# Performance work log

Hardware: AMD Instinct MI355X
Metric: run time of the kernel (lower is better)

## Reference

```python
import jax, jax.numpy as jnp
import numpy as np

B, T, TA = 16, 512, 1024
D_REG, D_AUD, HID, HEADS = 512, 512, 256, 4
NREG = 4  # mouth, left_eye, right_eye, nose (dict order)
N = NREG * B * T + B * TA  # total graph nodes


def _build_edges():
    # Faithful, vectorized version of build_graph's edge construction (phoneme_times=None).
    bs = np.arange(B)[:, None]
    ts = np.arange(T)[None, :]
    src, dst = [], []
    # cross-region same-timestep edges, all ordered pairs i != j (edge_attr 0)
    for i in range(NREG):
        for j in range(NREG):
            if i != j:
                n1 = i * B * T + bs * T + ts
                n2 = j * B * T + bs * T + ts
                src.append(n1.ravel()); dst.append(n2.ravel())
    # temporal edges within each region (edge_attr 1)
    tt = np.arange(T - 1)[None, :]
    for i in range(NREG):
        n1 = i * B * T + bs * T + tt
        src.append(n1.ravel()); dst.append((n1 + 1).ravel())
    # eye (region idx 1,2) -> audio alignment edges (edge_attr 3)
    t_aud = (np.arange(T)[None, :] * TA) // T
    audio_start = NREG * B * T
    for i in (1, 2):
        n_eye = i * B * T + bs * T + ts
        n_aud = audio_start + bs * TA + t_aud
        src.append(n_eye.ravel()); dst.append(np.broadcast_to(n_aud, (B, T)).ravel())
    # self loops (PyG GATConv default add_self_loops=True)
    loops = np.arange(N)
    src.append(loops); dst.append(loops)
    return np.concatenate(src).astype(np.int32), np.concatenate(dst).astype(np.int32)


def setup_inputs() -> dict:
    key = jax.random.key(0)
    ks = iter(jax.random.split(key, 48))
    def rn(shape, scale=1.0):
        return jax.random.normal(next(ks), shape, dtype=jnp.float32) * jnp.float32(scale)
    src_np, dst_np = _build_edges()
    inp = {
        'mouth': rn((B, T, D_REG)), 'left_eye': rn((B, T, D_REG)),
        'right_eye': rn((B, T, D_REG)), 'nose': rn((B, T, D_REG)),
        'audio_embeddings': rn((B, TA, D_AUD)),
    }
    s = 1.0 / np.sqrt(D_REG)
    for name in ['mouth', 'left_eye', 'right_eye', 'nose']:
        inp['w_' + name] = rn((D_REG, HID), s)
        inp['b_' + name] = jnp.zeros((HID,), jnp.float32)
    inp['w_audio'] = rn((D_AUD, HID), 1.0 / np.sqrt(D_AUD))
    inp['b_audio'] = jnp.zeros((HID,), jnp.float32)
    # GAT layers: layer 0 in=HID, layers 1,2 in=HID*HEADS; layers 0,1 concat, layer 2 averages heads
    dims_in = [HID, HID * HEADS, HID * HEADS]
    for l, din in enumerate(dims_in):
        concat = l < 2
        inp[f'W{l}'] = rn((din, HEADS * HID), 1.0 / np.sqrt(din))
        inp[f'as{l}'] = rn((HEADS, HID), 0.1)
        inp[f'ad{l}'] = rn((HEADS, HID), 0.1)
        inp[f'bias{l}'] = jnp.zeros((HEADS * HID,) if concat else (HID,), jnp.float32)
    inp['ln_g'] = jnp.ones((HID,), jnp.float32)
    inp['ln_b'] = jnp.zeros((HID,), jnp.float32)
    inp['src'] = jnp.asarray(src_np)
    inp['dst'] = jnp.asarray(dst_np)
    return inp


def _gat(x, W, a_s, a_d, bias, src, dst, concat):
    # PyG GATConv (eval mode): gather -> per-head attention softmax over dst -> scatter-add
    H, C = a_s.shape
    h = (x @ W).reshape(-1, H, C)                      # [N,H,C]
    alpha_s = jnp.sum(h * a_s, -1)                     # [N,H]
    alpha_d = jnp.sum(h * a_d, -1)                     # [N,H]
    e = jax.nn.leaky_relu(alpha_s[src] + alpha_d[dst], 0.2)  # [E,H]
    m = jax.ops.segment_max(e, dst, num_segments=N)
    ex = jnp.exp(e - m[dst])
    denom = jax.ops.segment_sum(ex, dst, num_segments=N)
    alpha = ex / (denom[dst] + jnp.float32(1e-16))
    out = jax.ops.segment_sum(h[src] * alpha[:, :, None], dst, num_segments=N)  # [N,H,C]
    out = out.reshape(-1, H * C) if concat else out.mean(1)
    return out + bias


def _forward(mouth, left_eye, right_eye, nose, audio_embeddings,
             w_mouth, b_mouth, w_left_eye, b_left_eye, w_right_eye, b_right_eye,
             w_nose, b_nose, w_audio, b_audio,
             W0, as0, ad0, bias0, W1, as1, ad1, bias1, W2, as2, ad2, bias2,
             ln_g, ln_b, src, dst):
    x = jnp.concatenate([
        (mouth @ w_mouth + b_mouth).reshape(B * T, HID),
        (left_eye @ w_left_eye + b_left_eye).reshape(B * T, HID),
        (right_eye @ w_right_eye + b_right_eye).reshape(B * T, HID),
        (nose @ w_nose + b_nose).reshape(B * T, HID),
        (audio_embeddings @ w_audio + b_audio).reshape(B * TA, HID),
    ], axis=0)                                          # [N,HID]
    x = _gat(x, W0, as0, ad0, bias0, src, dst, True)    # [N,HID*HEADS]
    x = _gat(x, W1, as1, ad1, bias1, src, dst, True)    # [N,HID*HEADS]
    x = _gat(x, W2, as2, ad2, bias2, src, dst, False)   # [N,HID]
    mu = x.mean(-1, keepdims=True)
    var = jnp.mean(jnp.square(x - mu), -1, keepdims=True)
    x = (x - mu) / jnp.sqrt(var + jnp.float32(1e-5)) * ln_g + ln_b
    nodes_pb = NREG * T + TA
    return x.reshape(B, nodes_pb, HID).mean(1)          # [B,HID]


def reference(mouth, left_eye, right_eye, nose, audio_embeddings,
              w_mouth, b_mouth, w_left_eye, b_left_eye, w_right_eye, b_right_eye,
              w_nose, b_nose, w_audio, b_audio,
              W0, as0, ad0, bias0, W1, as1, ad1, bias1, W2, as2, ad2, bias2,
              ln_g, ln_b, src, dst):
    return _forward(mouth, left_eye, right_eye, nose, audio_embeddings,
                    w_mouth, b_mouth, w_left_eye, b_left_eye, w_right_eye, b_right_eye,
                    w_nose, b_nose, w_audio, b_audio,
                    W0, as0, ad0, bias0, W1, as1, ad1, bias1, W2, as2, ad2, bias2,
                    ln_g, ln_b, src, dst)
```

## Files before the change

kernel.cpp:

```cpp
#include <hip/hip_runtime.h>


typedef unsigned short u16;
typedef unsigned int u32;
typedef __bf16 bf16x8 __attribute__((ext_vector_type(8)));
typedef float f32x4 __attribute__((ext_vector_type(4)));

#define ASYNC16(gp, lp)                                                        \
  __builtin_amdgcn_global_load_lds(                                            \
      (const __attribute__((address_space(1))) void*)(gp),                     \
      (__attribute__((address_space(3))) void*)(lp), 16, 0, 0)

__device__ __forceinline__ u16 f2bf(float f) {
  union { float f; u32 u; } v; v.f = f;
  u32 u = v.u + 0x7FFFu + ((v.u >> 16) & 1u);
  return (u16)(u >> 16);
}
__device__ __forceinline__ float bf2f(u16 x) {
  union { u32 u; float f; } v; v.u = ((u32)x) << 16;
  return v.f;
}
__device__ __forceinline__ float4 load_bf4(const u16* p) {
  ushort4 s = *(const ushort4*)p;
  float4 r; r.x = bf2f(s.x); r.y = bf2f(s.y); r.z = bf2f(s.z); r.w = bf2f(s.w);
  return r;
}
__device__ __forceinline__ float lrelu(float v) { return v > 0.f ? v : 0.2f * v; }
__device__ __forceinline__ float dot4(float4 a, float4 b) {
  return a.x * b.x + a.y * b.y + a.z * b.z + a.w * b.w;
}
__device__ __forceinline__ float wred(float v) {
#pragma unroll
  for (int off = 32; off; off >>= 1) v += __shfl_down(v, off);
  return v;
}
__device__ __forceinline__ float wredx(float v) {
#pragma unroll
  for (int off = 32; off; off >>= 1) v += __shfl_xor(v, off);
  return v;
}

struct PK { const float* W[8]; u16* P[8]; int KB[8]; int NN[8]; int st[9]; };
__global__ __launch_bounds__(256) void pack_kernel(PK p) {
  const int f = blockIdx.x * 4 + (threadIdx.x >> 6);
  const int lane = threadIdx.x & 63;
  int e = 0;
  while (f >= p.st[e + 1]) ++e;
  const int local = f - p.st[e];
  const int KB = p.KB[e], N = p.NN[e];
  const int nt = local / KB, kb = local % KB;
  const float* W = p.W[e] + (size_t)(kb * 32 + (lane >> 4) * 8) * N + nt * 16 + (lane & 15);
  u16* dst = p.P[e] + ((size_t)local * 64 + lane) * 8;
  u16 o[8];
#pragma unroll
  for (int j = 0; j < 8; ++j) o[j] = f2bf(W[(size_t)j * N]);
  *(uint4*)dst = *(uint4*)o;
}

__global__ __launch_bounds__(256) void gemm_kernel(
    const u16* __restrict__ A, const u16* __restrict__ Bp, u16* __restrict__ C,
    int K, int ldc) {
  __shared__ __align__(16) u16 As[128 * 32];
  const int KB = K >> 5;
  const int w = blockIdx.y * 8 + blockIdx.x;
  const int xcd = w & 7, m = w >> 3;
  const int blockCol = (m & 7) * 128;
  const int blockRow = ((m >> 3) * 8 + xcd) * 128;
  const int tid = threadIdx.x;
  const int wave = tid >> 6, lane = tid & 63;
  const int wr = (wave >> 1) * 64, wc = (wave & 1) * 64;
  const int lr = lane & 15, lq = lane >> 4;
  const int sRow = wave * 16 + (lane >> 2);
  const int sGc = (lane & 3) ^ ((sRow >> 1) & 3);
  const size_t aOff0 = (size_t)(blockRow + sRow) * K + sGc * 8;
  const size_t aOff1 = aOff0 + (size_t)64 * K;
  u16* asb0 = As + wave * 512;
  u16* asb1 = As + 2048 + wave * 512;

  const u16* Bn[4];
#pragma unroll
  for (int ni = 0; ni < 4; ++ni)
    Bn[ni] = Bp + ((size_t)(((blockCol + wc) >> 4) + ni) * KB) * 512 + lane * 8;

  f32x4 acc[4][4] = {};

  for (int k0 = 0; k0 < K; k0 += 32) {
    __syncthreads();
    ASYNC16(A + aOff0 + k0, asb0);
    ASYNC16(A + aOff1 + k0, asb1);
    bf16x8 bfr[4];
#pragma unroll
    for (int ni = 0; ni < 4; ++ni)
      bfr[ni] = *(const bf16x8*)(Bn[ni] + (size_t)k0 * 16);
    __syncthreads();
    bf16x8 af[4];
#pragma unroll
    for (int mi = 0; mi < 4; ++mi) {
      const int R = wr + mi * 16 + lr;
      const int cp = lq ^ ((R >> 1) & 3);
      af[mi] = *(const bf16x8*)(&As[R * 32 + cp * 8]);
    }
#pragma unroll
    for (int mi = 0; mi < 4; ++mi)
#pragma unroll
      for (int ni = 0; ni < 4; ++ni)
        acc[mi][ni] = __builtin_amdgcn_mfma_f32_16x16x32_bf16(af[mi], bfr[ni],
                                                              acc[mi][ni], 0, 0, 0);
  }
#pragma unroll
  for (int mi = 0; mi < 4; ++mi)
#pragma unroll
    for (int ni = 0; ni < 4; ++ni) {
      const int col = blockCol + wc + ni * 16 + lr;
#pragma unroll
      for (int r = 0; r < 4; ++r) {
        const int row = blockRow + wr + mi * 16 + lq * 4 + r;
        C[(size_t)row * ldc + col] = f2bf(acc[mi][ni][r]);
      }
    }
}

struct ProjArgs { const float* x[5]; const u16* w[5]; const float* b[5]; };
__global__ __launch_bounds__(256) void proj_kernel(ProjArgs pa,
                                                   u16* __restrict__ C) {
  __shared__ __align__(16) u16 As[128 * 32];
  const int blockRow = blockIdx.y * 128, blockCol = blockIdx.x * 128;
  const int reg = blockRow >= 32768 ? 4 : (blockRow >> 13);
  const int regBase = reg == 4 ? 32768 : reg * 8192;
  const float* Af = pa.x[reg] + (size_t)(blockRow - regBase) * 512;
  const u16* Bp = pa.w[reg];
  const int tid = threadIdx.x;
  const int wave = tid >> 6, lane = tid & 63;
  const int wr = (wave >> 1) * 64, wc = (wave & 1) * 64;
  const int lr = lane & 15, lq = lane >> 4;
  const int rr = tid >> 2;
  const int cphys = tid & 3;
  const int sGc = cphys ^ ((tid >> 3) & 3);

  const u16* Bn[4];
#pragma unroll
  for (int ni = 0; ni < 4; ++ni)
    Bn[ni] = Bp + ((size_t)(((blockCol + wc) >> 4) + ni) * 16) * 512 + lane * 8;

  f32x4 acc[4][4] = {};

  for (int k0 = 0; k0 < 512; k0 += 32) {
    __syncthreads();
    bf16x8 bfr[4];
#pragma unroll
    for (int ni = 0; ni < 4; ++ni)
      bfr[ni] = *(const bf16x8*)(Bn[ni] + (size_t)k0 * 16);
#pragma unroll
    for (int i = 0; i < 2; ++i) {
      const int row = i * 64 + rr;
      const float* ap = Af + (size_t)row * 512 + k0 + sGc * 8;
      float4 f0 = *(const float4*)(ap);
      float4 f1 = *(const float4*)(ap + 4);
      uint4 pk;
      pk.x = (u32)f2bf(f0.x) | ((u32)f2bf(f0.y) << 16);
      pk.y = (u32)f2bf(f0.z) | ((u32)f2bf(f0.w) << 16);
      pk.z = (u32)f2bf(f1.x) | ((u32)f2bf(f1.y) << 16);
      pk.w = (u32)f2bf(f1.z) | ((u32)f2bf(f1.w) << 16);
      *(uint4*)(&As[row * 32 + cphys * 8]) = pk;
    }
    __syncthreads();
    bf16x8 af[4];
#pragma unroll
    for (int mi = 0; mi < 4; ++mi) {
      const int R = wr + mi * 16 + lr;
      const int cp = lq ^ ((R >> 1) & 3);
      af[mi] = *(const bf16x8*)(&As[R * 32 + cp * 8]);
    }
#pragma unroll
    for (int mi = 0; mi < 4; ++mi)
#pragma unroll
      for (int ni = 0; ni < 4; ++ni)
        acc[mi][ni] = __builtin_amdgcn_mfma_f32_16x16x32_bf16(af[mi], bfr[ni],
                                                              acc[mi][ni], 0, 0, 0);
  }
  const float* bias = pa.b[reg];
#pragma unroll
  for (int mi = 0; mi < 4; ++mi)
#pragma unroll
    for (int ni = 0; ni < 4; ++ni) {
      const int col = blockCol + wc + ni * 16 + lr;
      const float bv = bias[col];
#pragma unroll
      for (int r = 0; r < 4; ++r) {
        const int row = blockRow + wr + mi * 16 + lq * 4 + r;
        C[(size_t)row * 256 + col] = f2bf(acc[mi][ni][r] + bv);
      }
    }
}

template <bool MEAN>
__global__ __launch_bounds__(256) void agg_kernel(
    const u16* __restrict__ h, const float* __restrict__ a_s,
    const float* __restrict__ a_d, const float* __restrict__ bias,
    void* __restrict__ out) {
  const int tid = threadIdx.x;
  const int head = tid >> 6, lane = tid & 63;
  const int c4 = tid * 4;
  const float4 sa = *(const float4*)(a_s + c4);
  const float4 da = *(const float4*)(a_d + c4);
  __shared__ float asL[4][4], adL[4][4], apL[4][4];
  __shared__ float alpha[4][4][5];

  if (blockIdx.x < 8192) {
    const int bt = blockIdx.x;
    const int t = bt & 511;
    const bool hasPrev = t > 0;
    float4 hv[4], hp[4];
#pragma unroll
    for (int r = 0; r < 4; ++r)
      hv[r] = load_bf4(h + (size_t)(r * 8192 + bt) * 1024 + c4);
    if (hasPrev) {
#pragma unroll
      for (int r = 0; r < 4; ++r)
        hp[r] = load_bf4(h + (size_t)(r * 8192 + bt - 1) * 1024 + c4);
    }
#pragma unroll
    for (int r = 0; r < 4; ++r) {
      float ss = wred(dot4(hv[r], sa));
      float dd = wred(dot4(hv[r], da));
      float sp = hasPrev ? wred(dot4(hp[r], sa)) : 0.f;
      if (lane == 0) { asL[r][head] = ss; adL[r][head] = dd; apL[r][head] = sp; }
    }
    __syncthreads();
    if (tid < 16) {
      const int j = tid >> 2, hh = tid & 3;
      const float ad = adL[j][hh];
      float e[5];
#pragma unroll
      for (int r = 0; r < 4; ++r) e[r] = lrelu(asL[r][hh] + ad);
      int cnt = 4;
      if (hasPrev) { e[4] = lrelu(apL[j][hh] + ad); cnt = 5; }
      float mx = e[0];
      for (int k = 1; k < cnt; ++k) mx = fmaxf(mx, e[k]);
      float s = 0.f, ex[5];
      for (int k = 0; k < cnt; ++k) { ex[k] = __expf(e[k] - mx); s += ex[k]; }
      const float inv = 1.f / (s + 1e-16f);
#pragma unroll
      for (int k = 0; k < 5; ++k) alpha[j][hh][k] = (k < cnt) ? ex[k] * inv : 0.f;
    }
    __syncthreads();
    if constexpr (!MEAN) {
      const float4 bv = *(const float4*)(bias + c4);
      u16* ob = (u16*)out;
#pragma unroll
      for (int j = 0; j < 4; ++j) {
        const float* al = &alpha[j][head][0];
        float4 acc;
        acc.x = al[0] * hv[0].x + al[1] * hv[1].x + al[2] * hv[2].x + al[3] * hv[3].x;
        acc.y = al[0] * hv[0].y + al[1] * hv[1].y + al[2] * hv[2].y + al[3] * hv[3].y;
        acc.z = al[0] * hv[0].z + al[1] * hv[1].z + al[2] * hv[2].z + al[3] * hv[3].z;
        acc.w = al[0] * hv[0].w + al[1] * hv[1].w + al[2] * hv[2].w + al[3] * hv[3].w;
        if (hasPrev) {
          const float a4 = al[4];
          acc.x += a4 * hp[j].x; acc.y += a4 * hp[j].y;
          acc.z += a4 * hp[j].z; acc.w += a4 * hp[j].w;
        }
        ushort4 o;
        o.x = f2bf(acc.x + bv.x); o.y = f2bf(acc.y + bv.y);
        o.z = f2bf(acc.z + bv.z); o.w = f2bf(acc.w + bv.w);
        *(ushort4*)(ob + (size_t)(j * 8192 + bt) * 1024 + c4) = o;
      }
    } else {
      __shared__ float red[4][1024];
#pragma unroll
      for (int j = 0; j < 4; ++j) {
        const float* al = &alpha[j][head][0];
        float4 acc;
        acc.x = al[0] * hv[0].x + al[1] * hv[1].x + al[2] * hv[2].x + al[3] * hv[3].x;
        acc.y = al[0] * hv[0].y + al[1] * hv[1].y + al[2] * hv[2].y + al[3] * hv[3].y;
        acc.z = al[0] * hv[0].z + al[1] * hv[1].z + al[2] * hv[2].z + al[3] * hv[3].z;
        acc.w = al[0] * hv[0].w + al[1] * hv[1].w + al[2] * hv[2].w + al[3] * hv[3].w;
        if (hasPrev) {
          const float a4 = al[4];
          acc.x += a4 * hp[j].x; acc.y += a4 * hp[j].y;
          acc.z += a4 * hp[j].z; acc.w += a4 * hp[j].w;
        }
        *(float4*)(&red[j][c4]) = acc;
      }
      __syncthreads();
      const float bb = bias[tid];
      float* of = (float*)out;
#pragma unroll
      for (int j = 0; j < 4; ++j)
        of[(size_t)(j * 8192 + bt) * 256 + tid] =
            0.25f * (red[j][tid] + red[j][tid + 256] + red[j][tid + 512] +
                     red[j][tid + 768]) + bb;
    }
  } else {
    const int idx = blockIdx.x - 8192;
    const int ta = idx & 1023;
    const int node = 32768 + idx;
    const bool even = ((ta & 1) == 0);
    float4 v = load_bf4(h + (size_t)node * 1024 + c4);
    if (even) {
      const int b = idx >> 10;
      const int tt = ta >> 1;
      const int le = 8192 + b * 512 + tt;
      const int re = 16384 + b * 512 + tt;
      float4 v1 = load_bf4(h + (size_t)le * 1024 + c4);
      float4 v2 = load_bf4(h + (size_t)re * 1024 + c4);
      float s0 = wred(dot4(v, sa));
      float s1 = wred(dot4(v1, sa));
      float s2 = wred(dot4(v2, sa));
      float d0 = wred(dot4(v, da));
      if (lane == 0) {
        asL[0][head] = s0; asL[1][head] = s1; asL[2][head] = s2; adL[0][head] = d0;
      }
      __syncthreads();
      if (tid < 4) {
        const float ad = adL[0][tid];
        float e0 = lrelu(asL[0][tid] + ad);
        float e1 = lrelu(asL[1][tid] + ad);
        float e2 = lrelu(asL[2][tid] + ad);
        float mx = fmaxf(e0, fmaxf(e1, e2));
        float x0 = __expf(e0 - mx), x1 = __expf(e1 - mx), x2 = __expf(e2 - mx);
        float inv = 1.f / (x0 + x1 + x2 + 1e-16f);
        alpha[0][tid][0] = x0 * inv; alpha[0][tid][1] = x1 * inv;
        alpha[0][tid][2] = x2 * inv;
      }
      __syncthreads();
      const float a0 = alpha[0][head][0], a1 = alpha[0][head][1], a2 = alpha[0][head][2];
      v.x = a0 * v.x + a1 * v1.x + a2 * v2.x;
      v.y = a0 * v.y + a1 * v1.y + a2 * v2.y;
      v.z = a0 * v.z + a1 * v1.z + a2 * v2.z;
      v.w = a0 * v.w + a1 * v1.w + a2 * v2.w;
    }
    if constexpr (!MEAN) {
      const float4 bv = *(const float4*)(bias + c4);
      ushort4 o;
      o.x = f2bf(v.x + bv.x); o.y = f2bf(v.y + bv.y);
      o.z = f2bf(v.z + bv.z); o.w = f2bf(v.w + bv.w);
      *(ushort4*)((u16*)out + (size_t)node * 1024 + c4) = o;
    } else {
      __shared__ float redA[1024];
      *(float4*)(&redA[c4]) = v;
      __syncthreads();
      float* of = (float*)out;
      of[(size_t)node * 256 + tid] =
          0.25f * (redA[tid] + redA[tid + 256] + redA[tid + 512] + redA[tid + 768]) +
          bias[tid];
    }
  }
}

__global__ __launch_bounds__(256) void ln_pool_kernel(
    const float* __restrict__ xf, const float* __restrict__ g,
    const float* __restrict__ bb, float* __restrict__ part) {
  const int tid = threadIdx.x;
  const int wave = tid >> 6, lane = tid & 63;
  const int node0 = blockIdx.x * 64 + wave * 16;
  const float4 g4 = *(const float4*)(g + lane * 4);
  const float4 b4 = *(const float4*)(bb + lane * 4);
  float4 acc = {0.f, 0.f, 0.f, 0.f};
  for (int i = 0; i < 16; ++i) {
    const float4 v = *(const float4*)(xf + (size_t)(node0 + i) * 256 + lane * 4);
    const float s = wredx(v.x + v.y + v.z + v.w);
    const float q = wredx(v.x * v.x + v.y * v.y + v.z * v.z + v.w * v.w);
    const float mean = s * (1.f / 256.f);
    const float var = q * (1.f / 256.f) - mean * mean;
    const float rstd = rsqrtf(var + 1e-5f);
    acc.x += (v.x - mean) * rstd * g4.x + b4.x;
    acc.y += (v.y - mean) * rstd * g4.y + b4.y;
    acc.z += (v.z - mean) * rstd * g4.z + b4.z;
    acc.w += (v.w - mean) * rstd * g4.w + b4.w;
  }
  *(float4*)(part + (size_t)(blockIdx.x * 4 + wave) * 256 + lane * 4) = acc;
}

__global__ __launch_bounds__(256) void pool2_kernel(const float* __restrict__ part,
                                                    float* __restrict__ out) {
  const int chunk = blockIdx.x;
  const int c = threadIdx.x;
  float s = 0.f;
  for (int i = 0; i < 192; ++i) s += part[(size_t)(chunk * 192 + i) * 256 + c];
  out[chunk * 256 + c] = s * (1.f / 3072.f);
}

extern "C" void kernel_launch(void* const* d_in, const int* in_sizes, int n_in,
                              void* d_out, int out_size, void* d_ws, size_t ws_size,
                              hipStream_t stream) {
  const float* x_reg[4] = {(const float*)d_in[0], (const float*)d_in[1],
                           (const float*)d_in[2], (const float*)d_in[3]};
  const float* audio = (const float*)d_in[4];
  const float* w_reg[4] = {(const float*)d_in[5], (const float*)d_in[7],
                           (const float*)d_in[9], (const float*)d_in[11]};
  const float* b_reg[4] = {(const float*)d_in[6], (const float*)d_in[8],
                           (const float*)d_in[10], (const float*)d_in[12]};
  const float* w_aud = (const float*)d_in[13];
  const float* b_aud = (const float*)d_in[14];
  const float* Wl[3] = {(const float*)d_in[15], (const float*)d_in[19],
                        (const float*)d_in[23]};
  const float* as_in[3] = {(const float*)d_in[16], (const float*)d_in[20],
                           (const float*)d_in[24]};
  const float* ad_in[3] = {(const float*)d_in[17], (const float*)d_in[21],
                           (const float*)d_in[25]};
  const float* bias_l[3] = {(const float*)d_in[18], (const float*)d_in[22],
                            (const float*)d_in[26]};
  const float* ln_g = (const float*)d_in[27];
  const float* ln_b = (const float*)d_in[28];

  char* ws = (char*)d_ws;
  u16* h_bf = (u16*)ws;
  float* part = (float*)ws;
  u16* xb = (u16*)(ws + 100663296);
  float* xf = (float*)xb;
  u16* wt = (u16*)(ws + 201326592);

  u16* wtp[5];
  for (int r = 0; r < 5; ++r) wtp[r] = wt + (size_t)r * 131072;
  u16* wt0 = wt + 655360;
  u16* wt1 = wt + 917504;
  u16* wt2 = wt + 1966080;

  PK pk;
  for (int r = 0; r < 4; ++r) { pk.W[r] = w_reg[r]; pk.P[r] = wtp[r]; pk.KB[r] = 16; pk.NN[r] = 256; }
  pk.W[4] = w_aud; pk.P[4] = wtp[4]; pk.KB[4] = 16; pk.NN[4] = 256;
  pk.W[5] = Wl[0]; pk.P[5] = wt0; pk.KB[5] = 8;  pk.NN[5] = 1024;
  pk.W[6] = Wl[1]; pk.P[6] = wt1; pk.KB[6] = 32; pk.NN[6] = 1024;
  pk.W[7] = Wl[2]; pk.P[7] = wt2; pk.KB[7] = 32; pk.NN[7] = 1024;
  pk.st[0] = 0;
  {
    const int nfr[8] = {256, 256, 256, 256, 256, 512, 2048, 2048};
    int acc = 0;
    for (int e = 0; e < 8; ++e) { acc += nfr[e]; pk.st[e + 1] = acc; }
  }
  pack_kernel<<<pk.st[8] / 4, 256, 0, stream>>>(pk);

  ProjArgs pa;
  for (int r = 0; r < 4; ++r) { pa.x[r] = x_reg[r]; pa.w[r] = wtp[r]; pa.b[r] = b_reg[r]; }
  pa.x[4] = audio; pa.w[4] = wtp[4]; pa.b[4] = b_aud;
  proj_kernel<<<dim3(2, 384), 256, 0, stream>>>(pa, xb);

  const u16* wl[3] = {wt0, wt1, wt2};
  const int Kl[3] = {256, 1024, 1024};
  for (int l = 0; l < 3; ++l) {
    gemm_kernel<<<dim3(8, 384), 256, 0, stream>>>(xb, wl[l], h_bf, Kl[l], 1024);
    if (l < 2)
      agg_kernel<false><<<24576, 256, 0, stream>>>(h_bf, as_in[l], ad_in[l],
                                                   bias_l[l], xb);
    else
      agg_kernel<true><<<24576, 256, 0, stream>>>(h_bf, as_in[l], ad_in[l],
                                                  bias_l[l], xf);
  }

  ln_pool_kernel<<<768, 256, 0, stream>>>(xf, ln_g, ln_b, part);
  pool2_kernel<<<16, 256, 0, stream>>>(part, (float*)d_out);
}
```

Measured before the change: 694.1 us.

## Write aggregation output in MFMA-packed layout and add LDS-free packed GEMM

The aggregation kernel for layers 0 and 1 now writes its bf16 output directly in the MFMA fragment-packed layout, and a new GEMM kernel reads A and B fragments straight from global memory with no LDS staging. Block indices in the aggregation kernel are also remapped so neighbouring blocks spread across XCDs. The aim is to remove the shared-memory staging and synchronisation in the K=1024 GEMMs. In exchange the new GEMM has no LDS reuse or software prefetch, so it relies on cache hits and may be latency bound, and the aggregation writes are scattered 8-byte stores.

```diff
diff --git a/kernel.cpp b/kernel.cpp
--- a/kernel.cpp
+++ b/kernel.cpp
@@ -55,6 +55,62 @@
 #pragma unroll
   for (int j = 0; j < 8; ++j) o[j] = f2bf(W[(size_t)j * N]);
   *(uint4*)dst = *(uint4*)o;
+}
+
+__global__ __launch_bounds__(256) void gemm_packed_kernel(
+    const u16* __restrict__ Ap, const u16* __restrict__ Bp, u16* __restrict__ C) {
+  const int KB = 32;
+  const int w = blockIdx.y * 8 + blockIdx.x;
+  const int xcd = w & 7, m = w >> 3;
+  const int blockCol = (m & 7) * 128;
+  const int blockRow = ((m >> 3) * 8 + xcd) * 128;
+  const int tid = threadIdx.x;
+  const int wave = tid >> 6, lane = tid & 63;
+  const int wr = (wave >> 1) * 64, wc = (wave & 1) * 64;
+  const int lr = lane & 15, lq = lane >> 4;
+
+  const u16* Ab[4];
+  const u16* Bb[4];
+#pragma unroll
+  for (int mi = 0; mi < 4; ++mi) {
+    const int mt = ((blockRow + wr) >> 4) + mi;
+    Ab[mi] = Ap + ((size_t)mt * KB * 64 + lane) * 8;
+  }
+#pragma unroll
+  for (int ni = 0; ni < 4; ++ni) {
+    const int nt = ((blockCol + wc) >> 4) + ni;
+    Bb[ni] = Bp + ((size_t)nt * KB * 64 + lane) * 8;
+  }
+
+  f32x4 acc[4][4] = {};
+
+#pragma unroll 2
+  for (int kb = 0; kb < KB; ++kb) {
+    bf16x8 af[4], bfr[4];
+#pragma unroll
+    for (int mi = 0; mi < 4; ++mi)
+      af[mi] = *(const bf16x8*)(Ab[mi] + kb * 512);
+#pragma unroll
+    for (int ni = 0; ni < 4; ++ni)
+      bfr[ni] = *(const bf16x8*)(Bb[ni] + kb * 512);
+#pragma unroll
+    for (int mi = 0; mi < 4; ++mi)
+#pragma unroll
+      for (int ni = 0; ni < 4; ++ni)
+        acc[mi][ni] = __builtin_amdgcn_mfma_f32_16x16x32_bf16(af[mi], bfr[ni],
+                                                              acc[mi][ni], 0, 0, 0);
+  }
+#pragma unroll
+  for (int mi = 0; mi < 4; ++mi)
+#pragma unroll
+    for (int ni = 0; ni < 4; ++ni) {
+      const int col = blockCol + wc + ni * 16 + lr;
+#pragma unroll
+      for (int r = 0; r < 4; ++r) {
+        const int row = blockRow + wr + mi * 16 + lq * 4 + r;
+        C[(size_t)row * 1024 + col] = f2bf(acc[mi][ni][r]);
+      }
+    }
 }
 
 __global__ __launch_bounds__(256) void gemm_kernel(
@@ -203,11 +259,13 @@
   const int c4 = tid * 4;
   const float4 sa = *(const float4*)(a_s + c4);
   const float4 da = *(const float4*)(a_d + c4);
+  const int kb = c4 >> 5, q = (c4 >> 3) & 3, j0 = c4 & 7;
   __shared__ float asL[4][4], adL[4][4], apL[4][4];
   __shared__ float alpha[4][4][5];
 
   if (blockIdx.x < 8192) {
-    const int bt = blockIdx.x;
+    const int id = blockIdx.x;
+    const int bt = ((id & 7) << 10) | (id >> 3);
     const int t = bt & 511;
     const bool hasPrev = t > 0;
     float4 hv[4], hp[4];
@@ -247,6 +305,7 @@
     if constexpr (!MEAN) {
       const float4 bv = *(const float4*)(bias + c4);
       u16* ob = (u16*)out;
+      const int r = bt & 15;
 #pragma unroll
       for (int j = 0; j < 4; ++j) {
         const float* al = &alpha[j][head][0];
@@ -263,7 +322,8 @@
         ushort4 o;
         o.x = f2bf(acc.x + bv.x); o.y = f2bf(acc.y + bv.y);
         o.z = f2bf(acc.z + bv.z); o.w = f2bf(acc.w + bv.w);
-        *(ushort4*)(ob + (size_t)(j * 8192 + bt) * 1024 + c4) = o;
+        const int mt = j * 512 + (bt >> 4);
+        *(ushort4*)(ob + (((size_t)(mt * 32 + kb) * 64 + q * 16 + r) * 8 + j0)) = o;
       }
     } else {
       __shared__ float red[4][1024];
@@ -292,7 +352,8 @@
                      red[j][tid + 768]) + bb;
     }
   } else {
-    const int idx = blockIdx.x - 8192;
+    const int aid = blockIdx.x - 8192;
+    const int idx = ((aid & 7) << 11) | (aid >> 3);
     const int ta = idx & 1023;
     const int node = 32768 + idx;
     const bool even = ((ta & 1) == 0);
@@ -335,7 +396,9 @@
       ushort4 o;
       o.x = f2bf(v.x + bv.x); o.y = f2bf(v.y + bv.y);
       o.z = f2bf(v.z + bv.z); o.w = f2bf(v.w + bv.w);
-      *(ushort4*)((u16*)out + (size_t)node * 1024 + c4) = o;
+      const int mt = 2048 + (idx >> 4), r = idx & 15;
+      *(ushort4*)((u16*)out +
+                  (((size_t)(mt * 32 + kb) * 64 + q * 16 + r) * 8 + j0)) = o;
     } else {
       __shared__ float redA[1024];
       *(float4*)(&redA[c4]) = v;
@@ -436,17 +499,15 @@
   pa.x[4] = audio; pa.w[4] = wtp[4]; pa.b[4] = b_aud;
   proj_kernel<<<dim3(2, 384), 256, 0, stream>>>(pa, xb);
 
-  const u16* wl[3] = {wt0, wt1, wt2};
-  const int Kl[3] = {256, 1024, 1024};
-  for (int l = 0; l < 3; ++l) {
-    gemm_kernel<<<dim3(8, 384), 256, 0, stream>>>(xb, wl[l], h_bf, Kl[l], 1024);
-    if (l < 2)
-      agg_kernel<false><<<24576, 256, 0, stream>>>(h_bf, as_in[l], ad_in[l],
-                                                   bias_l[l], xb);
-    else
-      agg_kernel<true><<<24576, 256, 0, stream>>>(h_bf, as_in[l], ad_in[l],
-                                                  bias_l[l], xf);
-  }
+  gemm_kernel<<<dim3(8, 384), 256, 0, stream>>>(xb, wt0, h_bf, 256, 1024);
+  agg_kernel<false><<<24576, 256, 0, stream>>>(h_bf, as_in[0], ad_in[0],
+                                               bias_l[0], xb);
+  gemm_packed_kernel<<<dim3(8, 384), 256, 0, stream>>>(xb, wt1, h_bf);
+  agg_kernel<false><<<24576, 256, 0, stream>>>(h_bf, as_in[1], ad_in[1],
+                                               bias_l[1], xb);
+  gemm_packed_kernel<<<dim3(8, 384), 256, 0, stream>>>(xb, wt2, h_bf);
+  agg_kernel<true><<<24576, 256, 0, stream>>>(h_bf, as_in[2], ad_in[2],
+                                              bias_l[2], xf);
 
   ln_pool_kernel<<<768, 256, 0, stream>>>(xf, ln_g, ln_b, part);
   pool2_kernel<<<16, 256, 0, stream>>>(part, (float*)d_out);
```

Result: slower. 740.5 us (+6.7%).
